# Kernel tuning notes

Measured on AMD Instinct MI355X. Metric: run time of the kernel, lower is better.

## Reference

```python
import jax, jax.numpy as jnp
import numpy as np

K = 256       # num states
M = 2         # markov order
D = 256       # lemb_size
V = 50000     # ntypes (vocab)
T = 512
B = 256
Kp1 = K + 1
EPS = 1e-5
INIT = 0.1


def _layernorm(h, g, b):
    mu = h.mean(-1, keepdims=True)
    var = ((h - mu) ** 2).mean(-1, keepdims=True)
    return (h - mu) / jnp.sqrt(var + EPS) * g + b


def setup_inputs() -> dict:
    key = jax.random.key(0)
    ks = jax.random.split(key, 12)
    u = lambda k, shp: jax.random.uniform(k, shp, jnp.float32, -INIT, INIT)
    return {
        "x": jax.random.randint(ks[0], (T, B), 0, V, dtype=jnp.int32),
        "z": jax.random.randint(ks[1], (T, B), 0, K, dtype=jnp.int32),
        "lembs": u(ks[2], (K, D)),
        "tlembs": u(ks[3], (Kp1, D)),
        "dec_W": u(ks[4], (V, D)),
        "dec_b": jnp.zeros((V,), jnp.float32),
        "em_W": u(ks[5], (D, D)),
        "em_bias": jnp.zeros((D,), jnp.float32),
        "em_g": jnp.ones((D,), jnp.float32),
        "em_beta": jnp.zeros((D,), jnp.float32),
        "td_W": u(ks[6], (K, M * D)),
        "td_b": jnp.zeros((K,), jnp.float32),
        "tm_W": u(ks[7], (M * D, M * D)),
        "tm_bias": jnp.zeros((M * D,), jnp.float32),
        "tn_g": jnp.ones((M * D,), jnp.float32),
        "tn_beta": jnp.zeros((M * D,), jnp.float32),
    }


def reference(x, z, lembs, tlembs, dec_W, dec_b, em_W, em_bias, em_g, em_beta,
              td_W, td_b, tm_W, tm_bias, tn_g, tn_beta):
    # --- emission distribution: K x V log-normalized ---
    h = _layernorm(lembs + jax.nn.relu(lembs @ em_W.T + em_bias), em_g, em_beta)
    emdist = jax.nn.log_softmax(h @ dec_W.T + dec_b, axis=1)  # (K, V)

    # --- transition distribution: (Kp1^M, K) log-normalized ---
    # cartesian product of label embeddings, row-major: row r <-> (i_0,...,i_{M-1})
    idx = jnp.indices((Kp1,) * M).reshape(M, -1)                 # (M, Kp1^M)
    cat = tlembs[idx].transpose(1, 0, 2).reshape(-1, M * D)      # (Kp1^M, M*D)
    th = _layernorm(cat + jax.nn.relu(cat @ tm_W.T + tm_bias), tn_g, tn_beta)
    transdist = jax.nn.log_softmax(th @ td_W.T + td_b, axis=1)   # (Kp1^M, K)

    # --- log_joint ---
    xlps = emdist.T[x]                                           # (T, B, K)
    emlps = jnp.take_along_axis(xlps, z[..., None].astype(jnp.int32), axis=2)[..., 0].sum(0)  # (B,)

    zpad = jnp.concatenate([jnp.full((M, B), K, dtype=z.dtype), z], axis=0)  # (T+M, B)
    win = jnp.stack([zpad[m:m + T] for m in range(M + 1)], 0)    # (M+1, T, B)
    lin = win[0]
    for m in range(1, M):
        lin = lin * Kp1 + win[m]                                 # row index into (Kp1^M, K)
    trans_lps = transdist[lin, win[M]]                           # (T, B)
    return emlps + trans_lps.sum(0)                              # (B,)
```

## Files before the change

kernel.cpp:

```cpp
#include <hip/hip_runtime.h>

#define Kst 256
#define Dd 256
#define Vv 50000
#define VPAD 50176
#define Tt 512
#define Bb 256
#define KP1 257
#define MD 512
#define NROWS (KP1*KP1)
#define EPSf 1e-5f

#define VB2 196
#define VB3 (VB2*4)
#define NTR ((NROWS+31)/32)
#define GPER 56
#define GEM  16
#define NGRP 52
#define GRID (GPER*NGRP)

typedef __attribute__((ext_vector_type(8))) short short8;
typedef __attribute__((ext_vector_type(4))) float f32x4;
typedef __attribute__((ext_vector_type(4))) unsigned u32x4;
typedef __attribute__((ext_vector_type(2))) unsigned u32x2;

__device__ __forceinline__ unsigned short f2bf(float f) {
    unsigned u = __builtin_bit_cast(unsigned, f);
    unsigned r = (u + 0x7fffu + ((u >> 16) & 1u)) >> 16;
    return (unsigned short)r;
}
__device__ __forceinline__ float bf2f(unsigned short u) {
    return __builtin_bit_cast(float, ((unsigned)u) << 16);
}
__device__ __forceinline__ unsigned bfpack(float lo, float hi) {
    return __builtin_amdgcn_perm(__builtin_bit_cast(unsigned, hi),
                                 __builtin_bit_cast(unsigned, lo), 0x07060302u);
}
__device__ __forceinline__ unsigned f2bf2(float lo, float hi) {
    return (unsigned)f2bf(lo) | ((unsigned)f2bf(hi) << 16);
}

union HPU {
    struct { short ta[32][264]; float lsep[4][32][2]; float musig[32][2]; } g;
    struct { short pl[64][266]; } p;
};

__global__ __launch_bounds__(256) void k_hP(
    const float* __restrict__ lembs, const float* __restrict__ em_W,
    const float* __restrict__ em_bias, const float* __restrict__ em_g,
    const float* __restrict__ em_beta, unsigned short* __restrict__ h_bf,
    const float* __restrict__ tlembs, const float* __restrict__ tm_W,
    float* __restrict__ P0, float* __restrict__ P1,
    const float* __restrict__ td_W, const float* __restrict__ tn_g,
    const float* __restrict__ tn_beta, const float* __restrict__ td_b,
    unsigned short* __restrict__ tdwg_bf, float* __restrict__ Gt,
    float* __restrict__ Bt, const float* __restrict__ dec_W,
    unsigned short* __restrict__ dwP)
{
    __shared__ HPU su;
    int bid = blockIdx.x;
    int tid = threadIdx.x, lane = tid & 63, wv = tid >> 6;
    int l15 = lane & 15, q = lane >> 4;

    if (bid >= 108) {
        int vb2 = bid - 108;
        short (*pl)[266] = su.p.pl;
        for (int c = 0; c < 4; ++c) {
            if (c) __syncthreads();
            int base_row = vb2*256 + c*64;
            #pragma unroll 4
            for (int i = 0; i < 16; ++i) {
                int row = wv*16 + i;
                int grow = base_row + row; if (grow > Vv-1) grow = Vv-1;
                float4 f = ((const float4*)(dec_W + (size_t)grow*Dd))[lane];
                u32x2 w; w.x = bfpack(f.x, f.y); w.y = bfpack(f.z, f.w);
                *(u32x2*)&pl[row][lane*4] = w;
            }
            __syncthreads();
            #pragma unroll
            for (int i = 0; i < 8; ++i) {
                short8 val = *(const short8*)&pl[(lane & 15)*4 + wv][i*32 + (lane >> 4)*8];
                *(short8*)(dwP + ((size_t)vb2*8192 + (size_t)i*1024
                                  + (c*4 + wv)*64 + lane)*8) = val;
            }
        }
        return;
    }

    if (bid >= 44) {
        int c = (bid - 44)*4 + wv;
        const float4* w4 = (const float4*)(td_W + (size_t)c*MD);
        const float4* g4 = (const float4*)tn_g;
        const float4* b4 = (const float4*)tn_beta;
        float sg = 0.f, sb = 0.f;
        short8 o;
        #pragma unroll
        for (int u = 0; u < 2; ++u) {
            int j4 = lane*2 + u;
            float4 w = w4[j4], g = g4[j4], bt = b4[j4];
            sg += w.x*g.x + w.y*g.y + w.z*g.z + w.w*g.w;
            sb += w.x*bt.x + w.y*bt.y + w.z*bt.z + w.w*bt.w;
            o[u*4+0] = (short)f2bf(w.x*g.x);
            o[u*4+1] = (short)f2bf(w.y*g.y);
            o[u*4+2] = (short)f2bf(w.z*g.z);
            o[u*4+3] = (short)f2bf(w.w*g.w);
        }
        {
            int wvv = c >> 6, l15v = (c >> 2) & 15, ctv = c & 3;
            int ksv = lane >> 2, qv = lane & 3;
            *(short8*)(tdwg_bf +
                ((((size_t)wvv*16 + ksv)*4 + ctv)*64 + (qv*16 + l15v))*8) = o;
        }
        #pragma unroll
        for (int dd = 32; dd > 0; dd >>= 1) {
            sg += __shfl_xor(sg, dd);
            sb += __shfl_xor(sb, dd);
        }
        if (lane == 0) { Gt[c] = sg; Bt[c] = sb + td_b[c]; }
        return;
    }

    short (*ta)[264] = su.g.ta;
    float (*lsep)[32][2] = su.g.lsep;
    float (*musig)[2] = su.g.musig;

    int job, r0, cb, koff, BK;
    const float* Arow; const float* Brow;
    if (bid < 8) {
        job = 0; r0 = bid*32; cb = 0; koff = 0; BK = Dd;
        Arow = lembs; Brow = em_W;
    } else {
        int b2 = bid - 8;
        int half = b2 / 18;
        int b3 = b2 % 18;
        job = 1 + half;
        r0 = (b3 >> 1) * 32;
        cb = (b3 & 1) * 256;
        koff = half * 256; BK = MD;
        Arow = tlembs; Brow = tm_W;
    }

    {
        int row = tid >> 3, seg = (tid & 7) * 32;
        int r = r0 + row;
        if (r > 256) r = 256;
        const float4* s4 = (const float4*)(Arow + (size_t)r*Dd + seg);
        #pragma unroll
        for (int u = 0; u < 4; ++u) {
            float4 f0 = s4[u*2], f1 = s4[u*2+1];
            u32x4 pk;
            pk.x = bfpack(f0.x, f0.y);
            pk.y = bfpack(f0.z, f0.w);
            pk.z = bfpack(f1.x, f1.y);
            pk.w = bfpack(f1.z, f1.w);
            *(short8*)&ta[row][seg + u*8] = __builtin_bit_cast(short8, pk);
        }
    }
    __syncthreads();

    const float* bptr[4];
    #pragma unroll
    for (int ct = 0; ct < 4; ++ct) {
        int j = cb + wv*64 + ct*16 + l15;
        bptr[ct] = Brow + (size_t)j*BK + koff + q*8;
    }
    f32x4 acc[2][4];
    #pragma unroll
    for (int rt = 0; rt < 2; ++rt)
        #pragma unroll
        for (int ct = 0; ct < 4; ++ct)
            acc[rt][ct] = (f32x4){0.f,0.f,0.f,0.f};
    for (int ks = 0; ks < 8; ++ks) {
        short8 a0 = *(const short8*)&ta[ 0 + l15][ks*32 + q*8];
        short8 a1 = *(const short8*)&ta[16 + l15][ks*32 + q*8];
        short8 b[4];
        #pragma unroll
        for (int ct = 0; ct < 4; ++ct) {
            float4 f0 = *(const float4*)(bptr[ct] + ks*32);
            float4 f1 = *(const float4*)(bptr[ct] + ks*32 + 4);
            u32x4 pk;
            pk.x = bfpack(f0.x, f0.y);
            pk.y = bfpack(f0.z, f0.w);
            pk.z = bfpack(f1.x, f1.y);
            pk.w = bfpack(f1.z, f1.w);
            b[ct] = __builtin_bit_cast(short8, pk);
        }
        #pragma unroll
        for (int ct = 0; ct < 4; ++ct) {
            acc[0][ct] = __builtin_amdgcn_mfma_f32_16x16x32_bf16(a0, b[ct], acc[0][ct], 0,0,0);
            acc[1][ct] = __builtin_amdgcn_mfma_f32_16x16x32_bf16(a1, b[ct], acc[1][ct], 0,0,0);
        }
    }

    if (job != 0) {
        float* Pd = (job == 1) ? P0 : P1;
        #pragma unroll
        for (int rt = 0; rt < 2; ++rt) {
            #pragma unroll
            for (int reg = 0; reg < 4; ++reg) {
                int r = r0 + rt*16 + q*4 + reg;
                if (r < KP1) {
                    float* dst = Pd + (size_t)r*MD + cb + wv*64;
                    #pragma unroll
                    for (int ct = 0; ct < 4; ++ct)
                        dst[ct*16 + l15] = acc[rt][ct][reg];
                }
            }
        }
        return;
    }

    float bias_c[4];
    #pragma unroll
    for (int ct = 0; ct < 4; ++ct)
        bias_c[ct] = em_bias[wv*64 + ct*16 + l15];
    #pragma unroll
    for (int rt = 0; rt < 2; ++rt) {
        #pragma unroll
        for (int reg = 0; reg < 4; ++reg) {
            int r = r0 + rt*16 + q*4 + reg;
            #pragma unroll
            for (int ct = 0; ct < 4; ++ct) {
                float lv = lembs[(size_t)r*Dd + wv*64 + ct*16 + l15];
                acc[rt][ct][reg] = lv + fmaxf(acc[rt][ct][reg] + bias_c[ct], 0.f);
            }
        }
    }
    #pragma unroll
    for (int rt = 0; rt < 2; ++rt) {
        #pragma unroll
        for (int reg = 0; reg < 4; ++reg) {
            float s  = ((acc[rt][0][reg] + acc[rt][1][reg]) + (acc[rt][2][reg] + acc[rt][3][reg]));
            float ss = ((acc[rt][0][reg]*acc[rt][0][reg] + acc[rt][1][reg]*acc[rt][1][reg])
                      + (acc[rt][2][reg]*acc[rt][2][reg] + acc[rt][3][reg]*acc[rt][3][reg]));
            s  += __shfl_xor(s, 1);  ss += __shfl_xor(ss, 1);
            s  += __shfl_xor(s, 2);  ss += __shfl_xor(ss, 2);
            s  += __shfl_xor(s, 4);  ss += __shfl_xor(ss, 4);
            s  += __shfl_xor(s, 8);  ss += __shfl_xor(ss, 8);
            if (l15 == 0) {
                int rw = rt*16 + q*4 + reg;
                lsep[wv][rw][0] = s;
                lsep[wv][rw][1] = ss;
            }
        }
    }
    __syncthreads();
    if (tid < 32) {
        float s  = (lsep[0][tid][0] + lsep[1][tid][0]) + (lsep[2][tid][0] + lsep[3][tid][0]);
        float ss = (lsep[0][tid][1] + lsep[1][tid][1]) + (lsep[2][tid][1] + lsep[3][tid][1]);
        float mu = s * (1.f/Dd);
        musig[tid][0] = mu;
        musig[tid][1] = rsqrtf(ss*(1.f/Dd) - mu*mu + EPSf);
    }
    __syncthreads();
    float gl[4], bl[4];
    #pragma unroll
    for (int ct = 0; ct < 4; ++ct) {
        gl[ct] = em_g[wv*64 + ct*16 + l15];
        bl[ct] = em_beta[wv*64 + ct*16 + l15];
    }
    #pragma unroll
    for (int rt = 0; rt < 2; ++rt) {
        #pragma unroll
        for (int reg = 0; reg < 4; ++reg) {
            int rw = rt*16 + q*4 + reg;
            int r = r0 + rw;
            float mu = musig[rw][0], rs = musig[rw][1];
            unsigned short* dst = h_bf + (size_t)r*Dd + wv*64;
            #pragma unroll
            for (int ct = 0; ct < 4; ++ct)
                dst[ct*16 + l15] = f2bf((acc[rt][ct][reg] - mu)*rs*gl[ct] + bl[ct]);
        }
    }
}

union SMemU {
    struct { short hs[64][264]; } em;
    struct { short th[32][520]; float musig[32][2]; float lsep[4][32][2]; } tr;
};

__global__ __launch_bounds__(256, 4) void k_emtrans(
    const unsigned short* __restrict__ dwP, const float* __restrict__ dec_b,
    const unsigned short* __restrict__ h_bf, float* __restrict__ part,
    unsigned short* __restrict__ E2,
    const float* __restrict__ tlembs, const float* __restrict__ P0,
    const float* __restrict__ P1, const float* __restrict__ tm_bias,
    const short* __restrict__ tdwg_bf, const float* __restrict__ Gt,
    const float* __restrict__ Bt, float* __restrict__ lse_t,
    unsigned short* __restrict__ Td)
{
    __shared__ SMemU sm;
    int bid = blockIdx.x;
    int tid = threadIdx.x, lane = tid & 63, wv = tid >> 6;
    int l15 = lane & 15, q = lane >> 4;

    int grp = bid / GPER, rem = bid % GPER;
    if (rem < GEM) {
        int em_id = grp*GEM + rem;
        int xcd = em_id & 7, slot = em_id >> 3;
        int g2 = slot >> 2, kg = slot & 3;
        int vb = g2*8 + xcd;
        if (vb >= VB2) return;
        short (*hs)[264] = sm.em.hs;

        {
            int row = tid >> 2, c0 = (tid & 3) * 64;
            const short8* src = (const short8*)(h_bf + (size_t)(kg*64 + row)*Dd + c0);
            #pragma unroll
            for (int u = 0; u < 8; ++u)
                *(short8*)&hs[row][c0 + u*8] = src[u];
        }
        __syncthreads();

        f32x4 acc[4][4];
        #pragma unroll
        for (int mt = 0; mt < 4; ++mt)
            #pragma unroll
            for (int ct = 0; ct < 4; ++ct)
                acc[mt][ct] = (f32x4){0.f,0.f,0.f,0.f};

        const short8* bb8 = (const short8*)dwP + ((size_t)vb*8*16 + wv*4)*64 + lane;
        short8 Bf[3][4];
        #define LDB_EM(slot_, kk) { \
            Bf[slot_][0] = bb8[((kk)*16 + 0)*64]; \
            Bf[slot_][1] = bb8[((kk)*16 + 1)*64]; \
            Bf[slot_][2] = bb8[((kk)*16 + 2)*64]; \
            Bf[slot_][3] = bb8[((kk)*16 + 3)*64]; }
        LDB_EM(0, 0)
        LDB_EM(1, 1)
        #pragma unroll
        for (int ks = 0; ks < 8; ++ks) {
            if (ks < 6) LDB_EM((ks+2)%3, ks+2)
            short8 a[4];
            #pragma unroll
            for (int mt = 0; mt < 4; ++mt)
                a[mt] = *(const short8*)&hs[mt*16 + l15][ks*32 + q*8];
            __builtin_amdgcn_s_setprio(1);
            #pragma unroll
            for (int mt = 0; mt < 4; ++mt)
                #pragma unroll
                for (int ct = 0; ct < 4; ++ct)
                    acc[mt][ct] = __builtin_amdgcn_mfma_f32_16x16x32_bf16(a[mt], Bf[ks%3][ct], acc[mt][ct], 0,0,0);
            __builtin_amdgcn_s_setprio(0);
        }
        #undef LDB_EM

        int vcol[4]; bool vok[4];
        #pragma unroll
        for (int ct = 0; ct < 4; ++ct) {
            int v = vb*256 + wv*64 + l15*4 + ct;
            vok[ct] = (v < Vv);
            vcol[ct] = v < Vv ? v : Vv-1;
        }
        #pragma unroll
        for (int ct = 0; ct < 4; ++ct) {
            if (vok[ct]) {
                float db = dec_b[vcol[ct]];
                #pragma unroll
                for (int mt = 0; mt < 4; ++mt)
                    #pragma unroll
                    for (int reg = 0; reg < 4; ++reg)
                        acc[mt][ct][reg] += db;
            } else {
                #pragma unroll
                for (int mt = 0; mt < 4; ++mt)
                    #pragma unroll
                    for (int reg = 0; reg < 4; ++reg)
                        acc[mt][ct][reg] = -1e30f;
            }
        }
        #pragma unroll
        for (int mt = 0; mt < 4; ++mt) {
            #pragma unroll
            for (int reg = 0; reg < 4; ++reg) {
                int k = kg*64 + mt*16 + q*4 + reg;
                u32x2 p;
                p.x = f2bf2(acc[mt][0][reg], acc[mt][1][reg]);
                p.y = f2bf2(acc[mt][2][reg], acc[mt][3][reg]);
                *(u32x2*)(E2 + (size_t)k*VPAD + vb*256 + wv*64 + l15*4) = p;
            }
        }
        #pragma unroll
        for (int mt = 0; mt < 4; ++mt) {
            #pragma unroll
            for (int reg = 0; reg < 4; ++reg) {
                float m = fmaxf(fmaxf(acc[mt][0][reg], acc[mt][1][reg]),
                                fmaxf(acc[mt][2][reg], acc[mt][3][reg]));
                m = fmaxf(m, __shfl_xor(m, 1));
                m = fmaxf(m, __shfl_xor(m, 2));
                m = fmaxf(m, __shfl_xor(m, 4));
                m = fmaxf(m, __shfl_xor(m, 8));
                float s = __expf(acc[mt][0][reg] - m) + __expf(acc[mt][1][reg] - m)
                        + __expf(acc[mt][2][reg] - m) + __expf(acc[mt][3][reg] - m);
                s += __shfl_xor(s, 1);
                s += __shfl_xor(s, 2);
                s += __shfl_xor(s, 4);
                s += __shfl_xor(s, 8);
                if (l15 == 0) {
                    int k = kg*64 + mt*16 + q*4 + reg;
                    part[((size_t)k*VB3 + vb*4 + wv)*2]     = m;
                    part[((size_t)k*VB3 + vb*4 + wv)*2 + 1] = s;
                }
            }
        }
        return;
    }

    int tr_id = grp*(GPER-GEM) + (rem - GEM);
    if (tr_id >= NTR) return;
    short (*th)[520]   = sm.tr.th;
    float (*musig)[2]  = sm.tr.musig;
    float (*lsep)[32][2] = sm.tr.lsep;
    int r0 = tr_id * 32;

    {
        const float4* bias0 = (const float4*)tm_bias;
        const float4* bias1 = (const float4*)(tm_bias + 256);
        float4 c0 = bias0[lane], c1 = bias1[lane];
        int i0a[8], i1a[8];
        #pragma unroll
        for (int i = 0; i < 8; ++i) {
            int r = r0 + wv*8 + i; if (r >= NROWS) r = NROWS - 1;
            i0a[i] = r / KP1; i1a[i] = r - i0a[i]*KP1;
        }
        #define ROWBODY(i, A0, B0, T0, A1, B1, T1) { \
            int row = wv*8 + (i); \
            float v0 = (T0).x + fmaxf((A0).x+(B0).x+c0.x, 0.f); \
            float v1 = (T0).y + fmaxf((A0).y+(B0).y+c0.y, 0.f); \
            float v2 = (T0).z + fmaxf((A0).z+(B0).z+c0.z, 0.f); \
            float v3 = (T0).w + fmaxf((A0).w+(B0).w+c0.w, 0.f); \
            float v4 = (T1).x + fmaxf((A1).x+(B1).x+c1.x, 0.f); \
            float v5 = (T1).y + fmaxf((A1).y+(B1).y+c1.y, 0.f); \
            float v6 = (T1).z + fmaxf((A1).z+(B1).z+c1.z, 0.f); \
            float v7 = (T1).w + fmaxf((A1).w+(B1).w+c1.w, 0.f); \
            u32x2 p0; p0.x = bfpack(v0, v1); p0.y = bfpack(v2, v3); \
            u32x2 p1; p1.x = bfpack(v4, v5); p1.y = bfpack(v6, v7); \
            *(u32x2*)&th[row][lane*4]       = p0; \
            *(u32x2*)&th[row][256 + lane*4] = p1; \
            float s  = ((v0+v1)+(v2+v3)) + ((v4+v5)+(v6+v7)); \
            float ss = ((v0*v0+v1*v1)+(v2*v2+v3*v3)) + ((v4*v4+v5*v5)+(v6*v6+v7*v7)); \
            _Pragma("unroll") \
            for (int d = 1; d < 64; d <<= 1) { \
                s  += __shfl_xor(s, d); \
                ss += __shfl_xor(ss, d); \
            } \
            if (lane == 0) { \
                float mu = s * (1.f/MD); \
                musig[row][0] = mu; \
                musig[row][1] = rsqrtf(ss*(1.f/MD) - mu*mu + EPSf); \
            } }

        if (i0a[0] == i0a[7]) {
            float4 A0 = ((const float4*)(P0 + (size_t)i0a[0]*MD))[lane];
            float4 A1 = ((const float4*)(P0 + (size_t)i0a[0]*MD + 256))[lane];
            float4 T0 = ((const float4*)(tlembs + (size_t)i0a[0]*Dd))[lane];
            #pragma unroll
            for (int i = 0; i < 8; ++i) {
                float4 b0 = ((const float4*)(P1 + (size_t)i1a[i]*MD))[lane];
                float4 b1 = ((const float4*)(P1 + (size_t)i1a[i]*MD + 256))[lane];
                float4 t1 = ((const float4*)(tlembs + (size_t)i1a[i]*Dd))[lane];
                ROWBODY(i, A0, b0, T0, A1, b1, t1)
            }
        } else {
            #pragma unroll
            for (int i = 0; i < 8; ++i) {
                float4 A0 = ((const float4*)(P0 + (size_t)i0a[i]*MD))[lane];
                float4 A1 = ((const float4*)(P0 + (size_t)i0a[i]*MD + 256))[lane];
                float4 T0 = ((const float4*)(tlembs + (size_t)i0a[i]*Dd))[lane];
                float4 b0 = ((const float4*)(P1 + (size_t)i1a[i]*MD))[lane];
                float4 b1 = ((const float4*)(P1 + (size_t)i1a[i]*MD + 256))[lane];
                float4 t1 = ((const float4*)(tlembs + (size_t)i1a[i]*Dd))[lane];
                ROWBODY(i, A0, b0, T0, A1, b1, t1)
            }
        }
        #undef ROWBODY
    }
    __syncthreads();

    f32x4 acc[2][4];
    #pragma unroll
    for (int rt = 0; rt < 2; ++rt)
        #pragma unroll
        for (int ct = 0; ct < 4; ++ct)
            acc[rt][ct] = (f32x4){0.f, 0.f, 0.f, 0.f};
    const short* bb = tdwg_bf + (size_t)wv*32768 + (size_t)lane*8;
    short8 Bf[3][4];
    #define LDB_TR(slot_, kk) { const short* nxt = bb + (size_t)(kk)*2048; \
        Bf[slot_][0] = *(const short8*)(nxt); \
        Bf[slot_][1] = *(const short8*)(nxt + 512); \
        Bf[slot_][2] = *(const short8*)(nxt + 1024); \
        Bf[slot_][3] = *(const short8*)(nxt + 1536); }
    LDB_TR(0, 0)
    LDB_TR(1, 1)
    #pragma unroll
    for (int ks = 0; ks < 16; ++ks) {
        if (ks < 14) LDB_TR((ks+2)%3, ks+2)
        int ko = ks*32 + q*8;
        short8 a0 = *(const short8*)&th[ 0 + l15][ko];
        short8 a1 = *(const short8*)&th[16 + l15][ko];
        __builtin_amdgcn_s_setprio(1);
        acc[0][0] = __builtin_amdgcn_mfma_f32_16x16x32_bf16(a0, Bf[ks%3][0], acc[0][0], 0,0,0);
        acc[1][0] = __builtin_amdgcn_mfma_f32_16x16x32_bf16(a1, Bf[ks%3][0], acc[1][0], 0,0,0);
        acc[0][1] = __builtin_amdgcn_mfma_f32_16x16x32_bf16(a0, Bf[ks%3][1], acc[0][1], 0,0,0);
        acc[1][1] = __builtin_amdgcn_mfma_f32_16x16x32_bf16(a1, Bf[ks%3][1], acc[1][1], 0,0,0);
        acc[0][2] = __builtin_amdgcn_mfma_f32_16x16x32_bf16(a0, Bf[ks%3][2], acc[0][2], 0,0,0);
        acc[1][2] = __builtin_amdgcn_mfma_f32_16x16x32_bf16(a1, Bf[ks%3][2], acc[1][2], 0,0,0);
        acc[0][3] = __builtin_amdgcn_mfma_f32_16x16x32_bf16(a0, Bf[ks%3][3], acc[0][3], 0,0,0);
        acc[1][3] = __builtin_amdgcn_mfma_f32_16x16x32_bf16(a1, Bf[ks%3][3], acc[1][3], 0,0,0);
        __builtin_amdgcn_s_setprio(0);
    }
    #undef LDB_TR

    float4 Gc = *(const float4*)(Gt + wv*64 + l15*4);
    float4 Bc = *(const float4*)(Bt + wv*64 + l15*4);
    #pragma unroll
    for (int rt = 0; rt < 2; ++rt) {
        #pragma unroll
        for (int reg = 0; reg < 4; ++reg) {
            int rw = rt*16 + q*4 + reg;
            float mu = musig[rw][0], rs = musig[rw][1];
            float e0 = rs*(acc[rt][0][reg] - mu*Gc.x) + Bc.x;
            float e1 = rs*(acc[rt][1][reg] - mu*Gc.y) + Bc.y;
            float e2 = rs*(acc[rt][2][reg] - mu*Gc.z) + Bc.z;
            float e3 = rs*(acc[rt][3][reg] - mu*Gc.w) + Bc.w;
            long r = (long)r0 + rw;
            if (r < NROWS) {
                u32x2 p;
                p.x = f2bf2(e0, e1);
                p.y = f2bf2(e2, e3);
                *(u32x2*)(Td + (size_t)r*Kst + wv*64 + l15*4) = p;
            }
            float m = fmaxf(fmaxf(e0, e1), fmaxf(e2, e3));
            m = fmaxf(m, __shfl_xor(m, 1));
            m = fmaxf(m, __shfl_xor(m, 2));
            m = fmaxf(m, __shfl_xor(m, 4));
            m = fmaxf(m, __shfl_xor(m, 8));
            float s = __expf(e0 - m) + __expf(e1 - m) + __expf(e2 - m) + __expf(e3 - m);
            s += __shfl_xor(s, 1);
            s += __shfl_xor(s, 2);
            s += __shfl_xor(s, 4);
            s += __shfl_xor(s, 8);
            if (l15 == 0) {
                lsep[wv][rw][0] = m;
                lsep[wv][rw][1] = s;
            }
        }
    }
    __syncthreads();
    if (tid < 32) {
        int r = r0 + tid;
        if (r < NROWS) {
            float m0 = lsep[0][tid][0], m1 = lsep[1][tid][0];
            float m2 = lsep[2][tid][0], m3 = lsep[3][tid][0];
            float mg = fmaxf(fmaxf(m0, m1), fmaxf(m2, m3));
            float s = lsep[0][tid][1]*__expf(m0-mg) + lsep[1][tid][1]*__expf(m1-mg)
                    + lsep[2][tid][1]*__expf(m2-mg) + lsep[3][tid][1]*__expf(m3-mg);
            lse_t[r] = mg + logf(s);
        }
    }
}

__global__ __launch_bounds__(64) void k_em_comb3(
    const float* __restrict__ part, float* __restrict__ lse_em)
{
    int k = blockIdx.x, lane = threadIdx.x;
    float m = -1e30f, s = 0.f;
    for (int vb = lane; vb < VB3; vb += 64) {
        float m2 = part[((size_t)k*VB3+vb)*2], s2 = part[((size_t)k*VB3+vb)*2+1];
        if (m2 > m) { s = s*__expf(m - m2) + s2; m = m2; }
        else          s += s2*__expf(m2 - m);
    }
    #pragma unroll
    for (int d = 1; d < 64; d <<= 1) {
        float mo = __shfl_xor(m, d), so = __shfl_xor(s, d);
        float mn = fmaxf(m, mo);
        s = s*__expf(m - mn) + so*__expf(mo - mn);
        m = mn;
    }
    if (lane == 0) lse_em[k] = m + logf(s);
}

#define GT_CH 2
__global__ __launch_bounds__(256) void k_gather3(
    const int* __restrict__ x, const int* __restrict__ z,
    const unsigned short* __restrict__ E2, const float* __restrict__ lse_em,
    const unsigned short* __restrict__ Td, const float* __restrict__ lse_t,
    float* __restrict__ out)
{
    int b = threadIdx.x;
    int t0 = blockIdx.x * GT_CH;
    float accv = 0.f;
    #pragma unroll
    for (int u = 0; u < GT_CH; ++u) {
        int t = t0 + u;
        int zc = z[t*Bb + b];
        int xv = x[t*Bb + b];
        int i0 = (t >= 2) ? z[(t-2)*Bb + b] : Kst;
        int i1 = (t >= 1) ? z[(t-1)*Bb + b] : Kst;
        int lin = i0*KP1 + i1;
        accv += bf2f(E2[(size_t)zc*VPAD + xv]) - lse_em[zc]
              + bf2f(Td[(size_t)lin*Kst + zc]) - lse_t[lin];
    }
    atomicAdd(&out[b], accv);
}

extern "C" void kernel_launch(void* const* d_in, const int* in_sizes, int n_in,
                              void* d_out, int out_size, void* d_ws, size_t ws_size,
                              hipStream_t stream)
{
    const int*   x       = (const int*)  d_in[0];
    const int*   z       = (const int*)  d_in[1];
    const float* lembs   = (const float*)d_in[2];
    const float* tlembs  = (const float*)d_in[3];
    const float* dec_W   = (const float*)d_in[4];
    const float* dec_b   = (const float*)d_in[5];
    const float* em_W    = (const float*)d_in[6];
    const float* em_bias = (const float*)d_in[7];
    const float* em_g    = (const float*)d_in[8];
    const float* em_beta = (const float*)d_in[9];
    const float* td_W    = (const float*)d_in[10];
    const float* td_b    = (const float*)d_in[11];
    const float* tm_W    = (const float*)d_in[12];
    const float* tm_bias = (const float*)d_in[13];
    const float* tn_g    = (const float*)d_in[14];
    const float* tn_beta = (const float*)d_in[15];
    float* out = (float*)d_out;

    float* ws     = (float*)d_ws;
    float* P0     = ws;
    float* P1     = P0 + 131584;
    float* lse_em = P1 + 131584;
    float* part   = lse_em + 256;
    float* lse_t  = part + 401408;
    float* Gt     = lse_t + 66052;
    float* Bt     = Gt + 256;
    unsigned short* tdwg_bf = (unsigned short*)(Bt + 256);
    unsigned short* h_bf   = tdwg_bf + 131072;
    unsigned short* E2     = h_bf + 65536;
    unsigned short* Td     = E2 + (size_t)Kst*VPAD;
    unsigned short* dwP    = Td + (size_t)NROWS*Kst;

    hipMemsetAsync(out, 0, Bb*sizeof(float), stream);
    k_hP<<<108 + VB2, 256, 0, stream>>>(lembs, em_W, em_bias, em_g, em_beta, h_bf,
                                        tlembs, tm_W, P0, P1,
                                        td_W, tn_g, tn_beta, td_b, tdwg_bf, Gt, Bt,
                                        dec_W, dwP);
    k_emtrans<<<GRID, 256, 0, stream>>>(
        dwP, dec_b, h_bf, part, E2,
        tlembs, P0, P1, tm_bias, (const short*)tdwg_bf, Gt, Bt, lse_t, Td);
    k_em_comb3<<<Kst, 64, 0, stream>>>(part, lse_em);
    k_gather3<<<Tt/GT_CH, 256, 0, stream>>>(x, z, E2, lse_em, Td, lse_t, out);
}
```

Baseline: 213.1 us.

## Split dec_W packing, reorder emtrans blocks, drop setprio, replace atomics with partial sums

```diff
diff --git a/kernel.cpp b/kernel.cpp
--- a/kernel.cpp
+++ b/kernel.cpp
@@ -14,10 +14,7 @@
 #define VB2 196
 #define VB3 (VB2*4)
 #define NTR ((NROWS+31)/32)
-#define GPER 56
-#define GEM  16
-#define NGRP 52
-#define GRID (GPER*NGRP)
+#define EMB 800
 
 typedef __attribute__((ext_vector_type(8))) short short8;
 typedef __attribute__((ext_vector_type(4))) float f32x4;
@@ -63,26 +60,24 @@
     int l15 = lane & 15, q = lane >> 4;
 
     if (bid >= 108) {
-        int vb2 = bid - 108;
+        int pb = bid - 108;
+        int vb2 = pb >> 2, c = pb & 3;
         short (*pl)[266] = su.p.pl;
-        for (int c = 0; c < 4; ++c) {
-            if (c) __syncthreads();
-            int base_row = vb2*256 + c*64;
-            #pragma unroll 4
-            for (int i = 0; i < 16; ++i) {
-                int row = wv*16 + i;
-                int grow = base_row + row; if (grow > Vv-1) grow = Vv-1;
-                float4 f = ((const float4*)(dec_W + (size_t)grow*Dd))[lane];
-                u32x2 w; w.x = bfpack(f.x, f.y); w.y = bfpack(f.z, f.w);
-                *(u32x2*)&pl[row][lane*4] = w;
-            }
-            __syncthreads();
-            #pragma unroll
-            for (int i = 0; i < 8; ++i) {
-                short8 val = *(const short8*)&pl[(lane & 15)*4 + wv][i*32 + (lane >> 4)*8];
-                *(short8*)(dwP + ((size_t)vb2*8192 + (size_t)i*1024
-                                  + (c*4 + wv)*64 + lane)*8) = val;
-            }
+        int base_row = vb2*256 + c*64;
+        #pragma unroll 4
+        for (int i = 0; i < 16; ++i) {
+            int row = wv*16 + i;
+            int grow = base_row + row; if (grow > Vv-1) grow = Vv-1;
+            float4 f = ((const float4*)(dec_W + (size_t)grow*Dd))[lane];
+            u32x2 w; w.x = bfpack(f.x, f.y); w.y = bfpack(f.z, f.w);
+            *(u32x2*)&pl[row][lane*4] = w;
+        }
+        __syncthreads();
+        #pragma unroll
+        for (int i = 0; i < 8; ++i) {
+            short8 val = *(const short8*)&pl[(lane & 15)*4 + wv][i*32 + (lane >> 4)*8];
+            *(short8*)(dwP + ((size_t)vb2*8192 + (size_t)i*1024
+                              + (c*4 + wv)*64 + lane)*8) = val;
         }
         return;
     }
@@ -294,10 +289,8 @@
     int tid = threadIdx.x, lane = tid & 63, wv = tid >> 6;
     int l15 = lane & 15, q = lane >> 4;
 
-    int grp = bid / GPER, rem = bid % GPER;
-    if (rem < GEM) {
-        int em_id = grp*GEM + rem;
-        int xcd = em_id & 7, slot = em_id >> 3;
+    if (bid < EMB) {
+        int xcd = bid & 7, slot = bid >> 3;
         int g2 = slot >> 2, kg = slot & 3;
         int vb = g2*8 + xcd;
         if (vb >= VB2) return;
@@ -335,13 +328,11 @@
             #pragma unroll
             for (int mt = 0; mt < 4; ++mt)
                 a[mt] = *(const short8*)&hs[mt*16 + l15][ks*32 + q*8];
-            __builtin_amdgcn_s_setprio(1);
             #pragma unroll
             for (int mt = 0; mt < 4; ++mt)
                 #pragma unroll
                 for (int ct = 0; ct < 4; ++ct)
                     acc[mt][ct] = __builtin_amdgcn_mfma_f32_16x16x32_bf16(a[mt], Bf[ks%3][ct], acc[mt][ct], 0,0,0);
-            __builtin_amdgcn_s_setprio(0);
         }
         #undef LDB_EM
 
@@ -406,7 +397,7 @@
         return;
     }
 
-    int tr_id = grp*(GPER-GEM) + (rem - GEM);
+    int tr_id = bid - EMB;
     if (tr_id >= NTR) return;
     short (*th)[520]   = sm.tr.th;
     float (*musig)[2]  = sm.tr.musig;
@@ -498,7 +489,6 @@
         int ko = ks*32 + q*8;
         short8 a0 = *(const short8*)&th[ 0 + l15][ko];
         short8 a1 = *(const short8*)&th[16 + l15][ko];
-        __builtin_amdgcn_s_setprio(1);
         acc[0][0] = __builtin_amdgcn_mfma_f32_16x16x32_bf16(a0, Bf[ks%3][0], acc[0][0], 0,0,0);
         acc[1][0] = __builtin_amdgcn_mfma_f32_16x16x32_bf16(a1, Bf[ks%3][0], acc[1][0], 0,0,0);
         acc[0][1] = __builtin_amdgcn_mfma_f32_16x16x32_bf16(a0, Bf[ks%3][1], acc[0][1], 0,0,0);
@@ -507,7 +497,6 @@
         acc[1][2] = __builtin_amdgcn_mfma_f32_16x16x32_bf16(a1, Bf[ks%3][2], acc[1][2], 0,0,0);
         acc[0][3] = __builtin_amdgcn_mfma_f32_16x16x32_bf16(a0, Bf[ks%3][3], acc[0][3], 0,0,0);
         acc[1][3] = __builtin_amdgcn_mfma_f32_16x16x32_bf16(a1, Bf[ks%3][3], acc[1][3], 0,0,0);
-        __builtin_amdgcn_s_setprio(0);
     }
     #undef LDB_TR
 
@@ -580,19 +569,20 @@
     if (lane == 0) lse_em[k] = m + logf(s);
 }
 
-#define GT_CH 2
-__global__ __launch_bounds__(256) void k_gather3(
+__global__ __launch_bounds__(256) void k_gather5(
     const int* __restrict__ x, const int* __restrict__ z,
     const unsigned short* __restrict__ E2, const float* __restrict__ lse_em,
     const unsigned short* __restrict__ Td, const float* __restrict__ lse_t,
-    float* __restrict__ out)
+    float* __restrict__ gpart)
 {
-    int b = threadIdx.x;
-    int t0 = blockIdx.x * GT_CH;
+    int tid = threadIdx.x;
+    int bc = blockIdx.x & 3, tc = blockIdx.x >> 2;
+    int b_local = tid >> 2, tg = tid & 3;
+    int b = bc*64 + b_local;
     float accv = 0.f;
     #pragma unroll
-    for (int u = 0; u < GT_CH; ++u) {
-        int t = t0 + u;
+    for (int u = 0; u < 4; ++u) {
+        int t = tc*16 + tg*4 + u;
         int zc = z[t*Bb + b];
         int xv = x[t*Bb + b];
         int i0 = (t >= 2) ? z[(t-2)*Bb + b] : Kst;
@@ -601,7 +591,20 @@
         accv += bf2f(E2[(size_t)zc*VPAD + xv]) - lse_em[zc]
               + bf2f(Td[(size_t)lin*Kst + zc]) - lse_t[lin];
     }
-    atomicAdd(&out[b], accv);
+    accv += __shfl_xor(accv, 1);
+    accv += __shfl_xor(accv, 2);
+    if (tg == 0) gpart[tc*Bb + b] = accv;
+}
+
+__global__ __launch_bounds__(256) void k_fin(
+    const float* __restrict__ gpart, float* __restrict__ out)
+{
+    int b = threadIdx.x;
+    float s = 0.f;
+    #pragma unroll
+    for (int tc = 0; tc < 32; ++tc)
+        s += gpart[tc*Bb + b];
+    out[b] = s;
 }
 
 extern "C" void kernel_launch(void* const* d_in, const int* in_sizes, int n_in,
@@ -634,20 +637,21 @@
     float* lse_t  = part + 401408;
     float* Gt     = lse_t + 66052;
     float* Bt     = Gt + 256;
-    unsigned short* tdwg_bf = (unsigned short*)(Bt + 256);
+    float* gpart  = Bt + 256;
+    unsigned short* tdwg_bf = (unsigned short*)(gpart + 8192);
     unsigned short* h_bf   = tdwg_bf + 131072;
     unsigned short* E2     = h_bf + 65536;
     unsigned short* Td     = E2 + (size_t)Kst*VPAD;
     unsigned short* dwP    = Td + (size_t)NROWS*Kst;
 
-    hipMemsetAsync(out, 0, Bb*sizeof(float), stream);
-    k_hP<<<108 + VB2, 256, 0, stream>>>(lembs, em_W, em_bias, em_g, em_beta, h_bf,
+    k_hP<<<108 + 784, 256, 0, stream>>>(lembs, em_W, em_bias, em_g, em_beta, h_bf,
                                         tlembs, tm_W, P0, P1,
                                         td_W, tn_g, tn_beta, td_b, tdwg_bf, Gt, Bt,
                                         dec_W, dwP);
-    k_emtrans<<<GRID, 256, 0, stream>>>(
+    k_emtrans<<<EMB + NTR, 256, 0, stream>>>(
         dwP, dec_b, h_bf, part, E2,
         tlembs, P0, P1, tm_bias, (const short*)tdwg_bf, Gt, Bt, lse_t, Td);
     k_em_comb3<<<Kst, 64, 0, stream>>>(part, lse_em);
-    k_gather3<<<Tt/GT_CH, 256, 0, stream>>>(x, z, E2, lse_em, Td, lse_t, out);
-}
+    k_gather5<<<128, 256, 0, stream>>>(x, z, E2, lse_em, Td, lse_t, gpart);
+    k_fin<<<1, 256, 0, stream>>>(gpart, out);
+}
```

Measured after the change: 205.6 us. 1.04x faster.
